# Kernel optimization log

Hardware: AMD Instinct MI355X
Metric: run time of the kernel (lower is better)

Reference implementation:

```python
import jax, jax.numpy as jnp
import numpy as np

N = 50000
NEG_SLOPE = 0.2  # PyG GATConv default leaky_relu slope


def _gat_layer(x, src, dst, W, a_s, a_d, b):
    # x: [N, Fin]; W: [Fin, H*C]; a_s, a_d: [H, C]; b: [C]
    H, C = a_s.shape
    xp = (x @ W).reshape(N, H, C)                      # projected node features per head
    alpha_s = jnp.einsum('nhc,hc->nh', xp, a_s)        # [N, H]
    alpha_d = jnp.einsum('nhc,hc->nh', xp, a_d)        # [N, H]
    e = jax.nn.leaky_relu(alpha_s[src] + alpha_d[dst], NEG_SLOPE)  # [E, H]
    # segment softmax over incoming edges of each dst node
    m = jax.ops.segment_max(e, dst, num_segments=N)
    m = jnp.where(jnp.isfinite(m), m, 0.0)
    p = jnp.exp(e - jax.lax.stop_gradient(m)[dst])
    denom = jax.ops.segment_sum(p, dst, num_segments=N)
    alpha = p / denom[dst]                             # [E, H]
    # scatter-aggregate messages
    out = jax.ops.segment_sum(alpha[:, :, None] * xp[src], dst, num_segments=N)  # [N, H, C]
    return out.mean(axis=1) + b                        # concat=False -> mean over heads


def setup_inputs() -> dict:
    key = jax.random.key(0)
    ks = jax.random.split(key, 16)
    IN, HID, OUT, H = 128, 64, 40, 4
    E = 800000
    x = jax.random.normal(ks[0], (N, IN), dtype=jnp.float32)
    edge_index = jax.random.randint(ks[1], (2, E), 0, N, dtype=jnp.int64)

    def mk(kw, ka, fin, fout):
        s = 1.0 / np.sqrt(fin)
        W = jax.random.normal(kw, (fin, H * fout), dtype=jnp.float32) * s
        a_s = jax.random.normal(ka, (H, fout), dtype=jnp.float32) * 0.1
        a_d = jax.random.normal(jax.random.fold_in(ka, 1), (H, fout), dtype=jnp.float32) * 0.1
        b = jnp.zeros((fout,), dtype=jnp.float32)
        return W, a_s, a_d, b

    W1, as1, ad1, b1 = mk(ks[2], ks[3], IN, HID)
    W2, as2, ad2, b2 = mk(ks[4], ks[5], HID, HID)
    W3, as3, ad3, b3 = mk(ks[6], ks[7], HID, OUT)
    return dict(x=x, edge_index=edge_index,
                W1=W1, as1=as1, ad1=ad1, b1=b1,
                W2=W2, as2=as2, ad2=ad2, b2=b2,
                W3=W3, as3=as3, ad3=ad3, b3=b3)


def reference(x, edge_index, W1, as1, ad1, b1, W2, as2, ad2, b2, W3, as3, ad3, b3):
    # PyG GATConv adds self-loops by default
    loop = jnp.arange(N, dtype=edge_index.dtype)
    src = jnp.concatenate([edge_index[0], loop])
    dst = jnp.concatenate([edge_index[1], loop])
    h = jax.nn.relu(_gat_layer(x, src, dst, W1, as1, ad1, b1))   # dropout is identity in eval
    h = jax.nn.relu(_gat_layer(h, src, dst, W2, as2, ad2, b2))
    h = jax.nn.relu(_gat_layer(h, src, dst, W3, as3, ad3, b3))
    return jax.nn.log_softmax(h, axis=-1)
```

## Files before the change

kernel.cpp:

```cpp
#include <hip/hip_runtime.h>
#include <math.h>

#define NNODES 50000
#define NEG_SLOPE 0.2f

typedef unsigned short ushort8v __attribute__((ext_vector_type(8)));
typedef unsigned short ushort4v __attribute__((ext_vector_type(4)));
typedef short short8v __attribute__((ext_vector_type(8)));
typedef float f32x4 __attribute__((ext_vector_type(4)));
typedef float f32x2 __attribute__((ext_vector_type(2)));

__device__ __forceinline__ float bf2f(unsigned short u){ return __uint_as_float(((unsigned)u) << 16); }
__device__ __forceinline__ unsigned short f2bf(float f){
    unsigned u = __float_as_uint(f);
    u += 0x7fff + ((u >> 16) & 1);
    return (unsigned short)(u >> 16);
}

__global__ void init_kernel(const unsigned long long* __restrict__ e, int* __restrict__ flag,
                            int* __restrict__ deg, int N){
    if(blockIdx.x == 0 && threadIdx.x < 64){
        const unsigned long long v = e[threadIdx.x];
        const unsigned long long mask = __ballot(v >= (1ULL << 32));
        if(threadIdx.x == 0) *flag = (mask == 0ULL) ? 1 : 0;
    }
    for(int i = blockIdx.x * blockDim.x + threadIdx.x; i < N; i += gridDim.x * blockDim.x)
        deg[i] = 0;
}

__global__ void hist_kernel(const void* __restrict__ e, const int* __restrict__ flag,
                            int* __restrict__ deg, int E){
    const int i = blockIdx.x * blockDim.x + threadIdx.x;
    if(i < E){
        const int d = (*flag) ? (int)((const long long*)e)[E + i] : ((const int*)e)[E + i];
        atomicAdd(&deg[d], 1);
    }
}

__global__ __launch_bounds__(512) void scan1_kernel(const int* __restrict__ deg,
                                                    int* __restrict__ excl,
                                                    int* __restrict__ bsum, int n){
    __shared__ int sh[512];
    const int t = threadIdx.x;
    const int gid = blockIdx.x * 512 + t;
    const int v = (gid < n) ? deg[gid] : 0;
    sh[t] = v;
    __syncthreads();
    for(int off = 1; off < 512; off <<= 1){
        const int add = (t >= off) ? sh[t - off] : 0;
        __syncthreads();
        sh[t] += add;
        __syncthreads();
    }
    if(gid < n) excl[gid] = sh[t] - v;
    if(t == 511) bsum[blockIdx.x] = sh[511];
}

__global__ __launch_bounds__(128) void scan2_kernel(int* __restrict__ bsum, int nb){
    __shared__ int sh[128];
    const int t = threadIdx.x;
    const int v = (t < nb) ? bsum[t] : 0;
    sh[t] = v;
    __syncthreads();
    for(int off = 1; off < 128; off <<= 1){
        const int add = (t >= off) ? sh[t - off] : 0;
        __syncthreads();
        sh[t] += add;
        __syncthreads();
    }
    if(t < nb) bsum[t] = sh[t] - v;
}

__global__ void scan3_kernel(const int* __restrict__ excl, const int* __restrict__ bsum,
                             int* __restrict__ row_ptr, int* __restrict__ cursor,
                             int n, int E){
    const int gid = blockIdx.x * blockDim.x + threadIdx.x;
    if(gid < n){
        const int r = excl[gid] + bsum[gid >> 9];
        row_ptr[gid] = r;
        cursor[gid] = r;
    }
    if(gid == 0) row_ptr[n] = E;
}

__global__ void scatter_kernel(const void* __restrict__ e, const int* __restrict__ flag,
                               int* __restrict__ cursor, int* __restrict__ col, int E){
    const int i = blockIdx.x * blockDim.x + threadIdx.x;
    if(i < E){
        int s, d;
        if(*flag){ s = (int)((const long long*)e)[i]; d = (int)((const long long*)e)[E + i]; }
        else     { s = ((const int*)e)[i];            d = ((const int*)e)[E + i]; }
        const int pos = atomicAdd(&cursor[d], 1);
        col[pos] = s;
    }
}

__device__ __forceinline__ void emit_wt(const float* __restrict__ W, const float* __restrict__ a_s,
                                        const float* __restrict__ a_d, unsigned short* __restrict__ Wt,
                                        int K, int NC, int C, int id){
    const int n = id / K, k = id - n * K;
    float v;
    if(n < NC){
        v = W[(size_t)k * NC + n];
    } else {
        const int h = n - NC;
        const int hh = h & 3;
        const float* av = (h < 4) ? a_s : a_d;
        v = 0.f;
        for(int c = 0; c < C; c++) v += W[(size_t)k * NC + hh * C + c] * av[hh * C + c];
    }
    Wt[(size_t)n * K + k] = f2bf(v);
}

__global__ void prep_kernel(const float* __restrict__ x, unsigned short* __restrict__ xbf, int X4,
                            const float* __restrict__ W1, const float* __restrict__ as1, const float* __restrict__ ad1,
                            const float* __restrict__ W2, const float* __restrict__ as2, const float* __restrict__ ad2,
                            const float* __restrict__ W3, const float* __restrict__ as3, const float* __restrict__ ad3,
                            unsigned short* __restrict__ W1t, unsigned short* __restrict__ W2t,
                            unsigned short* __restrict__ W3t){
    int id = blockIdx.x * blockDim.x + threadIdx.x;
    if(id < X4){
        const float4 v = *(const float4*)&x[(size_t)id * 4];
        ushort4v o;
        o[0] = f2bf(v.x); o[1] = f2bf(v.y); o[2] = f2bf(v.z); o[3] = f2bf(v.w);
        *(ushort4v*)&xbf[(size_t)id * 4] = o;
        return;
    }
    id -= X4;
    if(id < 264 * 128){ emit_wt(W1, as1, ad1, W1t, 128, 256, 64, id); return; }
    id -= 264 * 128;
    if(id < 264 * 64){ emit_wt(W2, as2, ad2, W2t, 64, 256, 64, id); return; }
    id -= 264 * 64;
    if(id < 168 * 64){ emit_wt(W3, as3, ad3, W3t, 64, 160, 40, id); }
}

template<int K, int NC>
__global__ __launch_bounds__(256) void mfma_gemm_kernel(const unsigned short* __restrict__ A,
                                                        const unsigned short* __restrict__ Bt,
                                                        unsigned short* __restrict__ C,
                                                        f32x2* __restrict__ ea,
                                                        f32x2* __restrict__ ed,
                                                        int M){
    const int lane = threadIdx.x & 63;
    const int wave = threadIdx.x >> 6;
    const int quad = lane >> 4;
    const int l16 = lane & 15;
    const int bm = blockIdx.x * 64;
    const int bn = blockIdx.y * 64;
    const int nt = (blockIdx.y == 0) ? 5 : 4;
    const int m = min(bm + wave * 16 + l16, M - 1);
    const size_t arow = (size_t)m * K;

    f32x4 acc[5];
    #pragma unroll
    for(int t = 0; t < 5; t++) acc[t] = (f32x4){0,0,0,0};
    int cn[5];
    #pragma unroll
    for(int t = 0; t < 4; t++) cn[t] = min(bn + t * 16 + l16, NC - 1);
    cn[4] = NC + min(l16, 7);

    for(int k0 = 0; k0 < K; k0 += 32){
        const short8v a = *(const short8v*)&A[arow + k0 + quad * 8];
        #pragma unroll
        for(int t = 0; t < 5; t++){
            if(t < nt){
                const short8v b = *(const short8v*)&Bt[(size_t)cn[t] * K + k0 + quad * 8];
                acc[t] = __builtin_amdgcn_mfma_f32_16x16x32_bf16(a, b, acc[t], 0, 0, 0);
            }
        }
    }
    const int rbase = bm + wave * 16 + quad * 4;
    #pragma unroll
    for(int t = 0; t < 4; t++){
        const int c = bn + t * 16 + l16;
        if(c < NC){
            #pragma unroll
            for(int r = 0; r < 4; r++){
                const int row = rbase + r;
                if(row < M) C[(size_t)row * NC + c] = f2bf(acc[t][r]);
            }
        }
    }
    if(blockIdx.y == 0 && l16 < 8){
        const int h = l16 & 3;
        f32x2* dst = (l16 < 4) ? ea : ed;
        #pragma unroll
        for(int r = 0; r < 4; r++){
            const int row = rbase + r;
            if(row < M){
                const float v = acc[4][r];
                f32x2 e2 = {__expf(v), __expf(NEG_SLOPE * v)};
                dst[(size_t)row * 4 + h] = e2;
            }
        }
    }
}

template<int C, bool FINAL>
__global__ __launch_bounds__(256) void gather_kernel(const unsigned short* __restrict__ xp,
                                                     const int* __restrict__ row_ptr,
                                                     const int* __restrict__ col,
                                                     const f32x2* __restrict__ ea,
                                                     const f32x2* __restrict__ ed,
                                                     const float* __restrict__ bias,
                                                     void* __restrict__ outv){
    constexpr int HC = 4 * C;
    constexpr int LPE = HC / 8;
    __shared__ float sbuf[4][FINAL ? HC : 1];
    const int lane = threadIdx.x & 63;
    const int wave = threadIdx.x >> 6;
    const int n = blockIdx.x * 4 + wave;
    const int half = lane >> 5;
    const int hl = lane & 31;
    const bool active = hl < LPE;
    const int head = min((8 * hl) / C, 3);
    const int rs = row_ptr[n], re = row_ptr[n + 1];
    const int T = re - rs + 1;
    const f32x2 edh = ed[(size_t)n * 4 + head];
    const unsigned short* xpl = xp + 8 * hl;

    f32x2 acc2[4] = {{0,0},{0,0},{0,0},{0,0}};
    float denom = 0.f;
    int k = 0;
    for(; k + 8 <= T; k += 8){
        const int e0 = rs + k + half, e1 = e0 + 2, e2 = e0 + 4, e3 = e0 + 6;
        const int s0 = (e0 < re) ? col[e0] : n;
        const int s1 = (e1 < re) ? col[e1] : n;
        const int s2 = (e2 < re) ? col[e2] : n;
        const int s3 = (e3 < re) ? col[e3] : n;
        const f32x2 a0 = ea[(size_t)s0 * 4 + head];
        const f32x2 a1 = ea[(size_t)s1 * 4 + head];
        const f32x2 a2 = ea[(size_t)s2 * 4 + head];
        const f32x2 a3 = ea[(size_t)s3 * 4 + head];
        const float w0 = fmaxf(a0[0] * edh[0], a0[1] * edh[1]);
        const float w1 = fmaxf(a1[0] * edh[0], a1[1] * edh[1]);
        const float w2 = fmaxf(a2[0] * edh[0], a2[1] * edh[1]);
        const float w3 = fmaxf(a3[0] * edh[0], a3[1] * edh[1]);
        denom += (w0 + w1) + (w2 + w3);
        if(active){
            const uint4 u0 = *(const uint4*)&xpl[(size_t)s0 * HC];
            const uint4 u1 = *(const uint4*)&xpl[(size_t)s1 * HC];
            const uint4 u2 = *(const uint4*)&xpl[(size_t)s2 * HC];
            const uint4 u3 = *(const uint4*)&xpl[(size_t)s3 * HC];
            const f32x2 W0 = {w0, w0}, W1 = {w1, w1}, W2 = {w2, w2}, W3 = {w3, w3};
            acc2[0] += W0 * (f32x2){__uint_as_float(u0.x << 16), __uint_as_float(u0.x & 0xffff0000u)};
            acc2[1] += W0 * (f32x2){__uint_as_float(u0.y << 16), __uint_as_float(u0.y & 0xffff0000u)};
            acc2[2] += W0 * (f32x2){__uint_as_float(u0.z << 16), __uint_as_float(u0.z & 0xffff0000u)};
            acc2[3] += W0 * (f32x2){__uint_as_float(u0.w << 16), __uint_as_float(u0.w & 0xffff0000u)};
            acc2[0] += W1 * (f32x2){__uint_as_float(u1.x << 16), __uint_as_float(u1.x & 0xffff0000u)};
            acc2[1] += W1 * (f32x2){__uint_as_float(u1.y << 16), __uint_as_float(u1.y & 0xffff0000u)};
            acc2[2] += W1 * (f32x2){__uint_as_float(u1.z << 16), __uint_as_float(u1.z & 0xffff0000u)};
            acc2[3] += W1 * (f32x2){__uint_as_float(u1.w << 16), __uint_as_float(u1.w & 0xffff0000u)};
            acc2[0] += W2 * (f32x2){__uint_as_float(u2.x << 16), __uint_as_float(u2.x & 0xffff0000u)};
            acc2[1] += W2 * (f32x2){__uint_as_float(u2.y << 16), __uint_as_float(u2.y & 0xffff0000u)};
            acc2[2] += W2 * (f32x2){__uint_as_float(u2.z << 16), __uint_as_float(u2.z & 0xffff0000u)};
            acc2[3] += W2 * (f32x2){__uint_as_float(u2.w << 16), __uint_as_float(u2.w & 0xffff0000u)};
            acc2[0] += W3 * (f32x2){__uint_as_float(u3.x << 16), __uint_as_float(u3.x & 0xffff0000u)};
            acc2[1] += W3 * (f32x2){__uint_as_float(u3.y << 16), __uint_as_float(u3.y & 0xffff0000u)};
            acc2[2] += W3 * (f32x2){__uint_as_float(u3.z << 16), __uint_as_float(u3.z & 0xffff0000u)};
            acc2[3] += W3 * (f32x2){__uint_as_float(u3.w << 16), __uint_as_float(u3.w & 0xffff0000u)};
        }
    }
    for(; k + 2 <= T; k += 2){
        const int e = rs + k + half;
        const int s = (e < re) ? col[e] : n;
        const f32x2 a2 = ea[(size_t)s * 4 + head];
        const float wh = fmaxf(a2[0] * edh[0], a2[1] * edh[1]);
        denom += wh;
        if(active){
            const uint4 u = *(const uint4*)&xpl[(size_t)s * HC];
            const f32x2 w2 = {wh, wh};
            acc2[0] += w2 * (f32x2){__uint_as_float(u.x << 16), __uint_as_float(u.x & 0xffff0000u)};
            acc2[1] += w2 * (f32x2){__uint_as_float(u.y << 16), __uint_as_float(u.y & 0xffff0000u)};
            acc2[2] += w2 * (f32x2){__uint_as_float(u.z << 16), __uint_as_float(u.z & 0xffff0000u)};
            acc2[3] += w2 * (f32x2){__uint_as_float(u.w << 16), __uint_as_float(u.w & 0xffff0000u)};
        }
    }
    if(k < T && half == 0){
        const int e = rs + k;
        const int s = (e < re) ? col[e] : n;
        const f32x2 a2 = ea[(size_t)s * 4 + head];
        const float wh = fmaxf(a2[0] * edh[0], a2[1] * edh[1]);
        denom += wh;
        if(active){
            const uint4 u = *(const uint4*)&xpl[(size_t)s * HC];
            const f32x2 w2 = {wh, wh};
            acc2[0] += w2 * (f32x2){__uint_as_float(u.x << 16), __uint_as_float(u.x & 0xffff0000u)};
            acc2[1] += w2 * (f32x2){__uint_as_float(u.y << 16), __uint_as_float(u.y & 0xffff0000u)};
            acc2[2] += w2 * (f32x2){__uint_as_float(u.z << 16), __uint_as_float(u.z & 0xffff0000u)};
            acc2[3] += w2 * (f32x2){__uint_as_float(u.w << 16), __uint_as_float(u.w & 0xffff0000u)};
        }
    }
    #pragma unroll
    for(int p = 0; p < 4; p++){
        acc2[p][0] += __shfl_xor(acc2[p][0], 32);
        acc2[p][1] += __shfl_xor(acc2[p][1], 32);
    }
    denom += __shfl_xor(denom, 32);
    const float ih = 1.f / denom;
    float acc[8];
    #pragma unroll
    for(int p = 0; p < 4; p++){ acc[2*p] = acc2[p][0] * ih; acc[2*p+1] = acc2[p][1] * ih; }

    if(!FINAL){
        #pragma unroll
        for(int j = 0; j < 8; j++){
            acc[j] += __shfl_xor(acc[j], 8);
            acc[j] += __shfl_xor(acc[j], 16);
        }
        if(lane < 8){
            unsigned short* out = (unsigned short*)outv;
            ushort8v o;
            #pragma unroll
            for(int j = 0; j < 8; j++)
                o[j] = f2bf(fmaxf(acc[j] * 0.25f + bias[8 * lane + j], 0.f));
            *(ushort8v*)&out[(size_t)n * C + 8 * lane] = o;
        }
    } else {
        if(active && half == 0){
            #pragma unroll
            for(int j = 0; j < 8; j++) sbuf[wave][8 * hl + j] = acc[j];
        }
        __syncthreads();
        float* out = (float*)outv;
        float4 o = {0,0,0,0};
        if(lane < 10){
            const int c = 4 * lane;
            #pragma unroll
            for(int h = 0; h < 4; h++){
                o.x += sbuf[wave][h * 40 + c + 0];
                o.y += sbuf[wave][h * 40 + c + 1];
                o.z += sbuf[wave][h * 40 + c + 2];
                o.w += sbuf[wave][h * 40 + c + 3];
            }
            const float4 b4 = *(const float4*)&bias[c];
            o.x = fmaxf(o.x * 0.25f + b4.x, 0.f);
            o.y = fmaxf(o.y * 0.25f + b4.y, 0.f);
            o.z = fmaxf(o.z * 0.25f + b4.z, 0.f);
            o.w = fmaxf(o.w * 0.25f + b4.w, 0.f);
        }
        float lm = (lane < 10) ? fmaxf(fmaxf(o.x, o.y), fmaxf(o.z, o.w)) : -INFINITY;
        #pragma unroll
        for(int off = 8; off; off >>= 1) lm = fmaxf(lm, __shfl_xor(lm, off));
        float se = 0.f;
        if(lane < 10) se = __expf(o.x-lm) + __expf(o.y-lm) + __expf(o.z-lm) + __expf(o.w-lm);
        #pragma unroll
        for(int off = 8; off; off >>= 1) se += __shfl_xor(se, off);
        const float logZ = lm + logf(se);
        if(lane < 10){
            float4 r = {o.x - logZ, o.y - logZ, o.z - logZ, o.w - logZ};
            *(float4*)&out[(size_t)n * 40 + 4 * lane] = r;
        }
    }
}

extern "C" void kernel_launch(void* const* d_in, const int* in_sizes, int n_in,
                              void* d_out, int out_size, void* d_ws, size_t ws_size,
                              hipStream_t stream){
    const int N = NNODES;
    const int E = in_sizes[1] / 2;

    const float* x   = (const float*)d_in[0];
    const float* W1  = (const float*)d_in[2];
    const float* as1 = (const float*)d_in[3];
    const float* ad1 = (const float*)d_in[4];
    const float* b1  = (const float*)d_in[5];
    const float* W2  = (const float*)d_in[6];
    const float* as2 = (const float*)d_in[7];
    const float* ad2 = (const float*)d_in[8];
    const float* b2  = (const float*)d_in[9];
    const float* W3  = (const float*)d_in[10];
    const float* as3 = (const float*)d_in[11];
    const float* ad3 = (const float*)d_in[12];
    const float* b3  = (const float*)d_in[13];

    char* ws = (char*)d_ws;
    size_t off = 0;
    auto alloc = [&](size_t bytes) -> void* {
        void* p = ws + off;
        off = (off + bytes + 255) & ~(size_t)255;
        return p;
    };
    int*   flag    = (int*)  alloc(4);
    int*   row_ptr = (int*)  alloc((size_t)(N + 1) * 4);
    int*   colv    = (int*)  alloc((size_t)E * 4);
    int*   cursor  = (int*)  alloc((size_t)N * 4);
    int*   deg     = (int*)  alloc((size_t)N * 4);
    int*   excl    = (int*)  alloc((size_t)N * 4);
    int*   bsum    = (int*)  alloc(128 * 4);
    unsigned short* xp  = (unsigned short*)alloc((size_t)N * 256 * 2);
    unsigned short* xbf = (unsigned short*)alloc((size_t)N * 128 * 2);
    unsigned short* W1t = (unsigned short*)alloc((size_t)264 * 128 * 2);
    unsigned short* W2t = (unsigned short*)alloc((size_t)264 * 64 * 2);
    unsigned short* W3t = (unsigned short*)alloc((size_t)168 * 64 * 2);
    f32x2* eav     = (f32x2*)alloc((size_t)N * 4 * 8);
    f32x2* edv     = (f32x2*)alloc((size_t)N * 4 * 8);
    unsigned short* h = (unsigned short*)alloc((size_t)N * 64 * 2);
    (void)ws_size;

    const void* eraw = d_in[1];

    init_kernel<<<(N + 255) / 256, 256, 0, stream>>>((const unsigned long long*)eraw, flag, deg, N);
    hist_kernel<<<(E + 255) / 256, 256, 0, stream>>>(eraw, flag, deg, E);

    const int X4 = N * 128 / 4;
    const int prepTotal = X4 + 264 * 128 + 264 * 64 + 168 * 64;
    prep_kernel<<<(prepTotal + 255) / 256, 256, 0, stream>>>(x, xbf, X4,
                                                             W1, as1, ad1, W2, as2, ad2,
                                                             W3, as3, ad3, W1t, W2t, W3t);

    const int nbScan = (N + 511) / 512;
    scan1_kernel<<<nbScan, 512, 0, stream>>>(deg, excl, bsum, N);
    scan2_kernel<<<1, 128, 0, stream>>>(bsum, nbScan);
    scan3_kernel<<<(N + 255) / 256, 256, 0, stream>>>(excl, bsum, row_ptr, cursor, N, E);
    scatter_kernel<<<(E + 255) / 256, 256, 0, stream>>>(eraw, flag, cursor, colv, E);

    const int nodeBlocks = N / 4;
    const int mBlocks = (N + 63) / 64;

    mfma_gemm_kernel<128, 256><<<dim3(mBlocks, 4), 256, 0, stream>>>(xbf, W1t, xp, eav, edv, N);
    gather_kernel<64, false><<<nodeBlocks, 256, 0, stream>>>(xp, row_ptr, colv, eav, edv, b1, h);

    mfma_gemm_kernel<64, 256><<<dim3(mBlocks, 4), 256, 0, stream>>>(h, W2t, xp, eav, edv, N);
    gather_kernel<64, false><<<nodeBlocks, 256, 0, stream>>>(xp, row_ptr, colv, eav, edv, b2, h);

    mfma_gemm_kernel<64, 160><<<dim3(mBlocks, 3), 256, 0, stream>>>(h, W3t, xp, eav, edv, N);
    gather_kernel<40, true><<<nodeBlocks, 256, 0, stream>>>(xp, row_ptr, colv, eav, edv, b3, (float*)d_out);
}
```

Measured before the change: 462.9 us.

## Reorder GAT layers to aggregate raw inputs before projecting with head-mean folded weights

New measurement: 436.3 us. 5.7% less time.

```diff
diff --git a/kernel.cpp b/kernel.cpp
--- a/kernel.cpp
+++ b/kernel.cpp
@@ -10,7 +10,6 @@
 typedef float f32x4 __attribute__((ext_vector_type(4)));
 typedef float f32x2 __attribute__((ext_vector_type(2)));
 
-__device__ __forceinline__ float bf2f(unsigned short u){ return __uint_as_float(((unsigned)u) << 16); }
 __device__ __forceinline__ unsigned short f2bf(float f){
     unsigned u = __float_as_uint(f);
     u += 0x7fff + ((u >> 16) & 1);
@@ -95,29 +94,35 @@
     }
 }
 
-__device__ __forceinline__ void emit_wt(const float* __restrict__ W, const float* __restrict__ a_s,
+__device__ __forceinline__ void emit_wa(const float* __restrict__ W, const float* __restrict__ a_s,
                                         const float* __restrict__ a_d, unsigned short* __restrict__ Wt,
-                                        int K, int NC, int C, int id){
-    const int n = id / K, k = id - n * K;
-    float v;
-    if(n < NC){
-        v = W[(size_t)k * NC + n];
-    } else {
-        const int h = n - NC;
-        const int hh = h & 3;
-        const float* av = (h < 4) ? a_s : a_d;
-        v = 0.f;
-        for(int c = 0; c < C; c++) v += W[(size_t)k * NC + hh * C + c] * av[hh * C + c];
-    }
-    Wt[(size_t)n * K + k] = f2bf(v);
+                                        int Kin, int C, int id){
+    const int n = id / Kin, k = id - n * Kin;
+    float v = 0.f;
+    if(n < 8){
+        const int hh = n & 3;
+        const float* av = (n < 4) ? a_s : a_d;
+        for(int c = 0; c < C; c++) v += W[(size_t)k * (4 * C) + hh * C + c] * av[hh * C + c];
+    }
+    Wt[id] = f2bf(v);
+}
+
+__device__ __forceinline__ void emit_wc(const float* __restrict__ W, unsigned short* __restrict__ Wt,
+                                        int Kin, int C, int id){
+    const int c = id / (4 * Kin);
+    const int hk = id - c * (4 * Kin);
+    const int h = hk / Kin, k = hk - h * Kin;
+    const float v = (c < C) ? W[(size_t)k * (4 * C) + h * C + c] * 0.25f : 0.f;
+    Wt[id] = f2bf(v);
 }
 
 __global__ void prep_kernel(const float* __restrict__ x, unsigned short* __restrict__ xbf, int X4,
                             const float* __restrict__ W1, const float* __restrict__ as1, const float* __restrict__ ad1,
                             const float* __restrict__ W2, const float* __restrict__ as2, const float* __restrict__ ad2,
                             const float* __restrict__ W3, const float* __restrict__ as3, const float* __restrict__ ad3,
-                            unsigned short* __restrict__ W1t, unsigned short* __restrict__ W2t,
-                            unsigned short* __restrict__ W3t){
+                            unsigned short* __restrict__ Wa1, unsigned short* __restrict__ Wa2,
+                            unsigned short* __restrict__ Wa3, unsigned short* __restrict__ Wc1,
+                            unsigned short* __restrict__ Wc2, unsigned short* __restrict__ Wc3){
     int id = blockIdx.x * blockDim.x + threadIdx.x;
     if(id < X4){
         const float4 v = *(const float4*)&x[(size_t)id * 4];
@@ -127,229 +132,215 @@
         return;
     }
     id -= X4;
-    if(id < 264 * 128){ emit_wt(W1, as1, ad1, W1t, 128, 256, 64, id); return; }
-    id -= 264 * 128;
-    if(id < 264 * 64){ emit_wt(W2, as2, ad2, W2t, 64, 256, 64, id); return; }
-    id -= 264 * 64;
-    if(id < 168 * 64){ emit_wt(W3, as3, ad3, W3t, 64, 160, 40, id); }
-}
-
-template<int K, int NC>
-__global__ __launch_bounds__(256) void mfma_gemm_kernel(const unsigned short* __restrict__ A,
-                                                        const unsigned short* __restrict__ Bt,
-                                                        unsigned short* __restrict__ C,
-                                                        f32x2* __restrict__ ea,
-                                                        f32x2* __restrict__ ed,
-                                                        int M){
+    if(id < 16 * 128){ emit_wa(W1, as1, ad1, Wa1, 128, 64, id); return; }
+    id -= 16 * 128;
+    if(id < 16 * 64){ emit_wa(W2, as2, ad2, Wa2, 64, 64, id); return; }
+    id -= 16 * 64;
+    if(id < 16 * 64){ emit_wa(W3, as3, ad3, Wa3, 64, 40, id); return; }
+    id -= 16 * 64;
+    if(id < 64 * 512){ emit_wc(W1, Wc1, 128, 64, id); return; }
+    id -= 64 * 512;
+    if(id < 64 * 256){ emit_wc(W2, Wc2, 64, 64, id); return; }
+    id -= 64 * 256;
+    if(id < 48 * 256){ emit_wc(W3, Wc3, 64, 40, id); }
+}
+
+template<int K>
+__global__ __launch_bounds__(256) void agemm_kernel(const unsigned short* __restrict__ A,
+                                                    const unsigned short* __restrict__ Wa,
+                                                    float* __restrict__ ea, float* __restrict__ ed,
+                                                    int M){
     const int lane = threadIdx.x & 63;
     const int wave = threadIdx.x >> 6;
     const int quad = lane >> 4;
     const int l16 = lane & 15;
     const int bm = blockIdx.x * 64;
-    const int bn = blockIdx.y * 64;
-    const int nt = (blockIdx.y == 0) ? 5 : 4;
     const int m = min(bm + wave * 16 + l16, M - 1);
-    const size_t arow = (size_t)m * K;
-
-    f32x4 acc[5];
+    f32x4 acc = {0,0,0,0};
     #pragma unroll
-    for(int t = 0; t < 5; t++) acc[t] = (f32x4){0,0,0,0};
-    int cn[5];
-    #pragma unroll
-    for(int t = 0; t < 4; t++) cn[t] = min(bn + t * 16 + l16, NC - 1);
-    cn[4] = NC + min(l16, 7);
-
     for(int k0 = 0; k0 < K; k0 += 32){
-        const short8v a = *(const short8v*)&A[arow + k0 + quad * 8];
-        #pragma unroll
-        for(int t = 0; t < 5; t++){
-            if(t < nt){
-                const short8v b = *(const short8v*)&Bt[(size_t)cn[t] * K + k0 + quad * 8];
-                acc[t] = __builtin_amdgcn_mfma_f32_16x16x32_bf16(a, b, acc[t], 0, 0, 0);
-            }
-        }
-    }
-    const int rbase = bm + wave * 16 + quad * 4;
-    #pragma unroll
-    for(int t = 0; t < 4; t++){
-        const int c = bn + t * 16 + l16;
-        if(c < NC){
-            #pragma unroll
-            for(int r = 0; r < 4; r++){
-                const int row = rbase + r;
-                if(row < M) C[(size_t)row * NC + c] = f2bf(acc[t][r]);
-            }
-        }
-    }
-    if(blockIdx.y == 0 && l16 < 8){
+        const short8v a = *(const short8v*)&A[(size_t)m * K + k0 + quad * 8];
+        const short8v b = *(const short8v*)&Wa[(size_t)l16 * K + k0 + quad * 8];
+        acc = __builtin_amdgcn_mfma_f32_16x16x32_bf16(a, b, acc, 0, 0, 0);
+    }
+    if(l16 < 8){
         const int h = l16 & 3;
-        f32x2* dst = (l16 < 4) ? ea : ed;
+        float* dst = (l16 < 4) ? ea : ed;
+        const int rbase = bm + wave * 16 + quad * 4;
         #pragma unroll
         for(int r = 0; r < 4; r++){
             const int row = rbase + r;
             if(row < M){
-                const float v = acc[4][r];
-                f32x2 e2 = {__expf(v), __expf(NEG_SLOPE * v)};
-                dst[(size_t)row * 4 + h] = e2;
+                const float v = acc[r];
+                *(f32x2*)&dst[(size_t)row * 8 + 2 * h] = (f32x2){__expf(v), __expf(NEG_SLOPE * v)};
             }
         }
     }
 }
 
-template<int C, bool FINAL>
-__global__ __launch_bounds__(256) void gather_kernel(const unsigned short* __restrict__ xp,
+template<int K>
+__global__ __launch_bounds__(256) void gather_kernel(const unsigned short* __restrict__ X,
                                                      const int* __restrict__ row_ptr,
                                                      const int* __restrict__ col,
-                                                     const f32x2* __restrict__ ea,
-                                                     const f32x2* __restrict__ ed,
-                                                     const float* __restrict__ bias,
-                                                     void* __restrict__ outv){
-    constexpr int HC = 4 * C;
-    constexpr int LPE = HC / 8;
-    __shared__ float sbuf[4][FINAL ? HC : 1];
+                                                     const float* __restrict__ ea,
+                                                     const float* __restrict__ ed,
+                                                     unsigned short* __restrict__ g){
+    constexpr int CPL = K / 16;
+    constexpr int PAIRS = CPL / 2;
     const int lane = threadIdx.x & 63;
     const int wave = threadIdx.x >> 6;
     const int n = blockIdx.x * 4 + wave;
-    const int half = lane >> 5;
-    const int hl = lane & 31;
-    const bool active = hl < LPE;
-    const int head = min((8 * hl) / C, 3);
+    const int slot = lane >> 4;
+    const int pos = lane & 15;
     const int rs = row_ptr[n], re = row_ptr[n + 1];
     const int T = re - rs + 1;
-    const f32x2 edh = ed[(size_t)n * 4 + head];
-    const unsigned short* xpl = xp + 8 * hl;
-
-    f32x2 acc2[4] = {{0,0},{0,0},{0,0},{0,0}};
-    float denom = 0.f;
+    const float4 edA = *(const float4*)&ed[(size_t)n * 8];
+    const float4 edB = *(const float4*)&ed[(size_t)n * 8 + 4];
+
+    f32x2 acc[4][PAIRS];
+    #pragma unroll
+    for(int h = 0; h < 4; h++)
+        #pragma unroll
+        for(int p = 0; p < PAIRS; p++) acc[h][p] = (f32x2){0.f, 0.f};
+    float dnm[4] = {0.f, 0.f, 0.f, 0.f};
+
+    auto body = [&](int e){
+        const int s = (e < re) ? col[e] : n;
+        const float4 eaA = *(const float4*)&ea[(size_t)s * 8];
+        const float4 eaB = *(const float4*)&ea[(size_t)s * 8 + 4];
+        const float w0 = fmaxf(eaA.x * edA.x, eaA.y * edA.y);
+        const float w1 = fmaxf(eaA.z * edA.z, eaA.w * edA.w);
+        const float w2 = fmaxf(eaB.x * edB.x, eaB.y * edB.y);
+        const float w3 = fmaxf(eaB.z * edB.z, eaB.w * edB.w);
+        dnm[0] += w0; dnm[1] += w1; dnm[2] += w2; dnm[3] += w3;
+        unsigned u[PAIRS];
+        if constexpr(PAIRS == 2){
+            const uint2 t2 = *(const uint2*)&X[(size_t)s * K + pos * CPL];
+            u[0] = t2.x; u[1] = t2.y;
+        } else {
+            const uint4 t4 = *(const uint4*)&X[(size_t)s * K + pos * CPL];
+            u[0] = t4.x; u[1] = t4.y; u[2] = t4.z; u[3] = t4.w;
+        }
+        #pragma unroll
+        for(int p = 0; p < PAIRS; p++){
+            const f32x2 v = {__uint_as_float(u[p] << 16), __uint_as_float(u[p] & 0xffff0000u)};
+            acc[0][p] += (f32x2){w0, w0} * v;
+            acc[1][p] += (f32x2){w1, w1} * v;
+            acc[2][p] += (f32x2){w2, w2} * v;
+            acc[3][p] += (f32x2){w3, w3} * v;
+        }
+    };
+
     int k = 0;
-    for(; k + 8 <= T; k += 8){
-        const int e0 = rs + k + half, e1 = e0 + 2, e2 = e0 + 4, e3 = e0 + 6;
-        const int s0 = (e0 < re) ? col[e0] : n;
-        const int s1 = (e1 < re) ? col[e1] : n;
-        const int s2 = (e2 < re) ? col[e2] : n;
-        const int s3 = (e3 < re) ? col[e3] : n;
-        const f32x2 a0 = ea[(size_t)s0 * 4 + head];
-        const f32x2 a1 = ea[(size_t)s1 * 4 + head];
-        const f32x2 a2 = ea[(size_t)s2 * 4 + head];
-        const f32x2 a3 = ea[(size_t)s3 * 4 + head];
-        const float w0 = fmaxf(a0[0] * edh[0], a0[1] * edh[1]);
-        const float w1 = fmaxf(a1[0] * edh[0], a1[1] * edh[1]);
-        const float w2 = fmaxf(a2[0] * edh[0], a2[1] * edh[1]);
-        const float w3 = fmaxf(a3[0] * edh[0], a3[1] * edh[1]);
-        denom += (w0 + w1) + (w2 + w3);
-        if(active){
-            const uint4 u0 = *(const uint4*)&xpl[(size_t)s0 * HC];
-            const uint4 u1 = *(const uint4*)&xpl[(size_t)s1 * HC];
-            const uint4 u2 = *(const uint4*)&xpl[(size_t)s2 * HC];
-            const uint4 u3 = *(const uint4*)&xpl[(size_t)s3 * HC];
-            const f32x2 W0 = {w0, w0}, W1 = {w1, w1}, W2 = {w2, w2}, W3 = {w3, w3};
-            acc2[0] += W0 * (f32x2){__uint_as_float(u0.x << 16), __uint_as_float(u0.x & 0xffff0000u)};
-            acc2[1] += W0 * (f32x2){__uint_as_float(u0.y << 16), __uint_as_float(u0.y & 0xffff0000u)};
-            acc2[2] += W0 * (f32x2){__uint_as_float(u0.z << 16), __uint_as_float(u0.z & 0xffff0000u)};
-            acc2[3] += W0 * (f32x2){__uint_as_float(u0.w << 16), __uint_as_float(u0.w & 0xffff0000u)};
-            acc2[0] += W1 * (f32x2){__uint_as_float(u1.x << 16), __uint_as_float(u1.x & 0xffff0000u)};
-            acc2[1] += W1 * (f32x2){__uint_as_float(u1.y << 16), __uint_as_float(u1.y & 0xffff0000u)};
-            acc2[2] += W1 * (f32x2){__uint_as_float(u1.z << 16), __uint_as_float(u1.z & 0xffff0000u)};
-            acc2[3] += W1 * (f32x2){__uint_as_float(u1.w << 16), __uint_as_float(u1.w & 0xffff0000u)};
-            acc2[0] += W2 * (f32x2){__uint_as_float(u2.x << 16), __uint_as_float(u2.x & 0xffff0000u)};
-            acc2[1] += W2 * (f32x2){__uint_as_float(u2.y << 16), __uint_as_float(u2.y & 0xffff0000u)};
-            acc2[2] += W2 * (f32x2){__uint_as_float(u2.z << 16), __uint_as_float(u2.z & 0xffff0000u)};
-            acc2[3] += W2 * (f32x2){__uint_as_float(u2.w << 16), __uint_as_float(u2.w & 0xffff0000u)};
-            acc2[0] += W3 * (f32x2){__uint_as_float(u3.x << 16), __uint_as_float(u3.x & 0xffff0000u)};
-            acc2[1] += W3 * (f32x2){__uint_as_float(u3.y << 16), __uint_as_float(u3.y & 0xffff0000u)};
-            acc2[2] += W3 * (f32x2){__uint_as_float(u3.z << 16), __uint_as_float(u3.z & 0xffff0000u)};
-            acc2[3] += W3 * (f32x2){__uint_as_float(u3.w << 16), __uint_as_float(u3.w & 0xffff0000u)};
-        }
-    }
-    for(; k + 2 <= T; k += 2){
-        const int e = rs + k + half;
-        const int s = (e < re) ? col[e] : n;
-        const f32x2 a2 = ea[(size_t)s * 4 + head];
-        const float wh = fmaxf(a2[0] * edh[0], a2[1] * edh[1]);
-        denom += wh;
-        if(active){
-            const uint4 u = *(const uint4*)&xpl[(size_t)s * HC];
-            const f32x2 w2 = {wh, wh};
-            acc2[0] += w2 * (f32x2){__uint_as_float(u.x << 16), __uint_as_float(u.x & 0xffff0000u)};
-            acc2[1] += w2 * (f32x2){__uint_as_float(u.y << 16), __uint_as_float(u.y & 0xffff0000u)};
-            acc2[2] += w2 * (f32x2){__uint_as_float(u.z << 16), __uint_as_float(u.z & 0xffff0000u)};
-            acc2[3] += w2 * (f32x2){__uint_as_float(u.w << 16), __uint_as_float(u.w & 0xffff0000u)};
-        }
-    }
-    if(k < T && half == 0){
-        const int e = rs + k;
-        const int s = (e < re) ? col[e] : n;
-        const f32x2 a2 = ea[(size_t)s * 4 + head];
-        const float wh = fmaxf(a2[0] * edh[0], a2[1] * edh[1]);
-        denom += wh;
-        if(active){
-            const uint4 u = *(const uint4*)&xpl[(size_t)s * HC];
-            const f32x2 w2 = {wh, wh};
-            acc2[0] += w2 * (f32x2){__uint_as_float(u.x << 16), __uint_as_float(u.x & 0xffff0000u)};
-            acc2[1] += w2 * (f32x2){__uint_as_float(u.y << 16), __uint_as_float(u.y & 0xffff0000u)};
-            acc2[2] += w2 * (f32x2){__uint_as_float(u.z << 16), __uint_as_float(u.z & 0xffff0000u)};
-            acc2[3] += w2 * (f32x2){__uint_as_float(u.w << 16), __uint_as_float(u.w & 0xffff0000u)};
-        }
-    }
+    for(; k + 8 <= T; k += 8){ body(rs + k + slot); body(rs + k + 4 + slot); }
+    for(; k + 4 <= T; k += 4){ body(rs + k + slot); }
+    if(k < T && slot < T - k){ body(rs + k + slot); }
+
     #pragma unroll
-    for(int p = 0; p < 4; p++){
-        acc2[p][0] += __shfl_xor(acc2[p][0], 32);
-        acc2[p][1] += __shfl_xor(acc2[p][1], 32);
-    }
-    denom += __shfl_xor(denom, 32);
-    const float ih = 1.f / denom;
-    float acc[8];
+    for(int msk = 16; msk < 64; msk <<= 1){
+        #pragma unroll
+        for(int h = 0; h < 4; h++){
+            #pragma unroll
+            for(int p = 0; p < PAIRS; p++){
+                acc[h][p][0] += __shfl_xor(acc[h][p][0], msk);
+                acc[h][p][1] += __shfl_xor(acc[h][p][1], msk);
+            }
+            dnm[h] += __shfl_xor(dnm[h], msk);
+        }
+    }
+    if(lane < 16){
+        #pragma unroll
+        for(int h = 0; h < 4; h++){
+            const float sc = 1.f / dnm[h];
+            if constexpr(PAIRS == 2){
+                ushort4v o;
+                o[0] = f2bf(acc[h][0][0] * sc); o[1] = f2bf(acc[h][0][1] * sc);
+                o[2] = f2bf(acc[h][1][0] * sc); o[3] = f2bf(acc[h][1][1] * sc);
+                *(ushort4v*)&g[(size_t)n * (4 * K) + h * K + pos * CPL] = o;
+            } else {
+                ushort8v o;
+                #pragma unroll
+                for(int p = 0; p < 4; p++){
+                    o[2*p]   = f2bf(acc[h][p][0] * sc);
+                    o[2*p+1] = f2bf(acc[h][p][1] * sc);
+                }
+                *(ushort8v*)&g[(size_t)n * (4 * K) + h * K + pos * CPL] = o;
+            }
+        }
+    }
+}
+
+template<int KC, int NC, bool FINAL>
+__global__ __launch_bounds__(256) void pgemm_kernel(const unsigned short* __restrict__ A,
+                                                    const unsigned short* __restrict__ Bt,
+                                                    const float* __restrict__ bias,
+                                                    void* __restrict__ outv, int M){
+    constexpr int NT = (NC + 15) / 16;
+    const int lane = threadIdx.x & 63;
+    const int wave = threadIdx.x >> 6;
+    const int quad = lane >> 4;
+    const int l16 = lane & 15;
+    const int bm = blockIdx.x * 64;
+    const int m = min(bm + wave * 16 + l16, M - 1);
+    const size_t arow = (size_t)m * KC;
+
+    f32x4 acc[NT];
     #pragma unroll
-    for(int p = 0; p < 4; p++){ acc[2*p] = acc2[p][0] * ih; acc[2*p+1] = acc2[p][1] * ih; }
-
+    for(int t = 0; t < NT; t++) acc[t] = (f32x4){0,0,0,0};
+
+    for(int k0 = 0; k0 < KC; k0 += 32){
+        const short8v a = *(const short8v*)&A[arow + k0 + quad * 8];
+        #pragma unroll
+        for(int t = 0; t < NT; t++){
+            const short8v b = *(const short8v*)&Bt[(size_t)(t * 16 + l16) * KC + k0 + quad * 8];
+            acc[t] = __builtin_amdgcn_mfma_f32_16x16x32_bf16(a, b, acc[t], 0, 0, 0);
+        }
+    }
+    const int rbase = bm + wave * 16 + quad * 4;
     if(!FINAL){
-        #pragma unroll
-        for(int j = 0; j < 8; j++){
-            acc[j] += __shfl_xor(acc[j], 8);
-            acc[j] += __shfl_xor(acc[j], 16);
-        }
-        if(lane < 8){
-            unsigned short* out = (unsigned short*)outv;
-            ushort8v o;
-            #pragma unroll
-            for(int j = 0; j < 8; j++)
-                o[j] = f2bf(fmaxf(acc[j] * 0.25f + bias[8 * lane + j], 0.f));
-            *(ushort8v*)&out[(size_t)n * C + 8 * lane] = o;
+        unsigned short* out = (unsigned short*)outv;
+        #pragma unroll
+        for(int t = 0; t < NT; t++){
+            const int c = t * 16 + l16;
+            #pragma unroll
+            for(int r = 0; r < 4; r++){
+                const int row = rbase + r;
+                if(row < M) out[(size_t)row * NC + c] = f2bf(fmaxf(acc[t][r] + bias[c], 0.f));
+            }
         }
     } else {
-        if(active && half == 0){
-            #pragma unroll
-            for(int j = 0; j < 8; j++) sbuf[wave][8 * hl + j] = acc[j];
-        }
-        __syncthreads();
         float* out = (float*)outv;
-        float4 o = {0,0,0,0};
-        if(lane < 10){
-            const int c = 4 * lane;
-            #pragma unroll
-            for(int h = 0; h < 4; h++){
-                o.x += sbuf[wave][h * 40 + c + 0];
-                o.y += sbuf[wave][h * 40 + c + 1];
-                o.z += sbuf[wave][h * 40 + c + 2];
-                o.w += sbuf[wave][h * 40 + c + 3];
+        float o[NT][4];
+        #pragma unroll
+        for(int t = 0; t < NT; t++){
+            const int c = t * 16 + l16;
+            const bool valid = c < 40;
+            const float bc = valid ? bias[c] : 0.f;
+            #pragma unroll
+            for(int r = 0; r < 4; r++)
+                o[t][r] = valid ? fmaxf(acc[t][r] + bc, 0.f) : -INFINITY;
+        }
+        #pragma unroll
+        for(int r = 0; r < 4; r++){
+            float mx = o[0][r];
+            #pragma unroll
+            for(int t = 1; t < NT; t++) mx = fmaxf(mx, o[t][r]);
+            #pragma unroll
+            for(int off = 1; off < 16; off <<= 1) mx = fmaxf(mx, __shfl_xor(mx, off));
+            float se = 0.f;
+            #pragma unroll
+            for(int t = 0; t < NT; t++) se += (o[t][r] > -INFINITY) ? __expf(o[t][r] - mx) : 0.f;
+            #pragma unroll
+            for(int off = 1; off < 16; off <<= 1) se += __shfl_xor(se, off);
+            const float lz = mx + logf(se);
+            const int row = rbase + r;
+            if(row < M){
+                #pragma unroll
+                for(int t = 0; t < NT; t++){
+                    const int c = t * 16 + l16;
+                    if(c < 40) out[(size_t)row * 40 + c] = o[t][r] - lz;
+                }
             }
-            const float4 b4 = *(const float4*)&bias[c];
-            o.x = fmaxf(o.x * 0.25f + b4.x, 0.f);
-            o.y = fmaxf(o.y * 0.25f + b4.y, 0.f);
-            o.z = fmaxf(o.z * 0.25f + b4.z, 0.f);
-            o.w = fmaxf(o.w * 0.25f + b4.w, 0.f);
-        }
-        float lm = (lane < 10) ? fmaxf(fmaxf(o.x, o.y), fmaxf(o.z, o.w)) : -INFINITY;
-        #pragma unroll
-        for(int off = 8; off; off >>= 1) lm = fmaxf(lm, __shfl_xor(lm, off));
-        float se = 0.f;
-        if(lane < 10) se = __expf(o.x-lm) + __expf(o.y-lm) + __expf(o.z-lm) + __expf(o.w-lm);
-        #pragma unroll
-        for(int off = 8; off; off >>= 1) se += __shfl_xor(se, off);
-        const float logZ = lm + logf(se);
-        if(lane < 10){
-            float4 r = {o.x - logZ, o.y - logZ, o.z - logZ, o.w - logZ};
-            *(float4*)&out[(size_t)n * 40 + 4 * lane] = r;
         }
     }
 }
@@ -388,14 +379,17 @@
     int*   deg     = (int*)  alloc((size_t)N * 4);
     int*   excl    = (int*)  alloc((size_t)N * 4);
     int*   bsum    = (int*)  alloc(128 * 4);
-    unsigned short* xp  = (unsigned short*)alloc((size_t)N * 256 * 2);
     unsigned short* xbf = (unsigned short*)alloc((size_t)N * 128 * 2);
-    unsigned short* W1t = (unsigned short*)alloc((size_t)264 * 128 * 2);
-    unsigned short* W2t = (unsigned short*)alloc((size_t)264 * 64 * 2);
-    unsigned short* W3t = (unsigned short*)alloc((size_t)168 * 64 * 2);
-    f32x2* eav     = (f32x2*)alloc((size_t)N * 4 * 8);
-    f32x2* edv     = (f32x2*)alloc((size_t)N * 4 * 8);
-    unsigned short* h = (unsigned short*)alloc((size_t)N * 64 * 2);
+    unsigned short* Wa1 = (unsigned short*)alloc(16 * 128 * 2);
+    unsigned short* Wa2 = (unsigned short*)alloc(16 * 64 * 2);
+    unsigned short* Wa3 = (unsigned short*)alloc(16 * 64 * 2);
+    unsigned short* Wc1 = (unsigned short*)alloc((size_t)64 * 512 * 2);
+    unsigned short* Wc2 = (unsigned short*)alloc((size_t)64 * 256 * 2);
+    unsigned short* Wc3 = (unsigned short*)alloc((size_t)48 * 256 * 2);
+    float* eav     = (float*)alloc((size_t)N * 8 * 4);
+    float* edv     = (float*)alloc((size_t)N * 8 * 4);
+    unsigned short* g   = (unsigned short*)alloc((size_t)N * 512 * 2);
+    unsigned short* h   = (unsigned short*)alloc((size_t)N * 64 * 2);
     (void)ws_size;
 
     const void* eraw = d_in[1];
@@ -404,10 +398,10 @@
     hist_kernel<<<(E + 255) / 256, 256, 0, stream>>>(eraw, flag, deg, E);
 
     const int X4 = N * 128 / 4;
-    const int prepTotal = X4 + 264 * 128 + 264 * 64 + 168 * 64;
+    const int prepTotal = X4 + 16*128 + 16*64 + 16*64 + 64*512 + 64*256 + 48*256;
     prep_kernel<<<(prepTotal + 255) / 256, 256, 0, stream>>>(x, xbf, X4,
-                                                             W1, as1, ad1, W2, as2, ad2,
-                                                             W3, as3, ad3, W1t, W2t, W3t);
+                                                             W1, as1, ad1, W2, as2, ad2, W3, as3, ad3,
+                                                             Wa1, Wa2, Wa3, Wc1, Wc2, Wc3);
 
     const int nbScan = (N + 511) / 512;
     scan1_kernel<<<nbScan, 512, 0, stream>>>(deg, excl, bsum, N);
@@ -418,12 +412,15 @@
     const int nodeBlocks = N / 4;
     const int mBlocks = (N + 63) / 64;
 
-    mfma_gemm_kernel<128, 256><<<dim3(mBlocks, 4), 256, 0, stream>>>(xbf, W1t, xp, eav, edv, N);
-    gather_kernel<64, false><<<nodeBlocks, 256, 0, stream>>>(xp, row_ptr, colv, eav, edv, b1, h);
-
-    mfma_gemm_kernel<64, 256><<<dim3(mBlocks, 4), 256, 0, stream>>>(h, W2t, xp, eav, edv, N);
-    gather_kernel<64, false><<<nodeBlocks, 256, 0, stream>>>(xp, row_ptr, colv, eav, edv, b2, h);
-
-    mfma_gemm_kernel<64, 160><<<dim3(mBlocks, 3), 256, 0, stream>>>(h, W3t, xp, eav, edv, N);
-    gather_kernel<40, true><<<nodeBlocks, 256, 0, stream>>>(xp, row_ptr, colv, eav, edv, b3, (float*)d_out);
-}
+    agemm_kernel<128><<<mBlocks, 256, 0, stream>>>(xbf, Wa1, eav, edv, N);
+    gather_kernel<128><<<nodeBlocks, 256, 0, stream>>>(xbf, row_ptr, colv, eav, edv, g);
+    pgemm_kernel<512, 64, false><<<mBlocks, 256, 0, stream>>>(g, Wc1, b1, h, N);
+
+    agemm_kernel<64><<<mBlocks, 256, 0, stream>>>(h, Wa2, eav, edv, N);
+    gather_kernel<64><<<nodeBlocks, 256, 0, stream>>>(h, row_ptr, colv, eav, edv, g);
+    pgemm_kernel<256, 64, false><<<mBlocks, 256, 0, stream>>>(g, Wc2, b2, h, N);
+
+    agemm_kernel<64><<<mBlocks, 256, 0, stream>>>(h, Wa3, eav, edv, N);
+    gather_kernel<64><<<nodeBlocks, 256, 0, stream>>>(h, row_ptr, colv, eav, edv, g);
+    pgemm_kernel<256, 40, true><<<mBlocks, 256, 0, stream>>>(g, Wc3, b3, d_out, N);
+}
```
